# Optimization experiments

Measured on AMD Instinct MI355X. Metric: run time of the kernel, lower is better.

## Reference

```python
import jax, jax.numpy as jnp
import numpy as np
import math

B, T, C, H = 4, 4096, 1024, 16
D = C // H

def setup_inputs() -> dict:
    key = jax.random.key(0)
    k1, k2, k3, k4, k5 = jax.random.split(key, 5)
    s = 1.0 / math.sqrt(C)
    return {
        "x": jax.random.normal(k1, (B, T, C), dtype=jnp.float32),
        "W_qkv": jax.random.normal(k2, (C, 3 * C), dtype=jnp.float32) * s,
        "b_qkv": jax.random.normal(k3, (3 * C,), dtype=jnp.float32) * 0.01,
        "W_out": jax.random.normal(k4, (C, C), dtype=jnp.float32) * s,
        "b_out": jax.random.normal(k5, (C,), dtype=jnp.float32) * 0.01,
    }

def reference(x, W_qkv, b_qkv, W_out, b_out):
    qkv = x @ W_qkv + b_qkv                      # (B,T,3C)
    q, k, v = jnp.split(qkv, 3, axis=2)
    q = q.reshape(B, T, H, D)
    k = k.reshape(B, T, H, D)
    v = v.reshape(B, T, H, D)
    # attention over the HEAD axis per (B,T): scores (B,T,H,H)
    att = jnp.einsum('bthd,btgd->bthg', q, k) / math.sqrt(D)
    att = jax.nn.softmax(att, axis=-1)
    out = jnp.einsum('bthg,btgd->bthd', att, v)  # (B,T,H,D)
    out = out.reshape(B, T, C)
    return out @ W_out + b_out
```

## Files before the change

### kernel.cpp

```cpp
#include <hip/hip_runtime.h>
#include <cstdint>
#include <cstddef>

constexpr int Bc = 4;
constexpr int Tc = 4096;
constexpr int Cc = 1024;
constexpr int Hc = 16;
constexpr int Dc = 64;
constexpr int Mc = Bc * Tc;
constexpr int N1c = 3 * Cc;
constexpr int Kc = Cc;
constexpr int KBc = Kc / 32;

typedef __bf16 bf16x8 __attribute__((ext_vector_type(8)));
typedef float  f32x4  __attribute__((ext_vector_type(4)));
typedef __attribute__((address_space(1))) uint32_t gu32;
typedef __attribute__((address_space(3))) uint32_t lu32;

__device__ __forceinline__ float bf2f(unsigned short u) {
    return __uint_as_float(((unsigned)u) << 16);
}
__device__ __forceinline__ unsigned short f2bf(float f) {
    unsigned u = __float_as_uint(f);
    u += 0x7FFF + ((u >> 16) & 1);
    return (unsigned short)(u >> 16);
}

__device__ __forceinline__ void load_lds16(const void* g, void* l) {
    __builtin_amdgcn_global_load_lds((gu32*)(uintptr_t)g, (lu32*)(uintptr_t)l, 16, 0, 0);
}


__global__ __launch_bounds__(256) void prep_kernel(
    const float* __restrict__ x,    unsigned short* __restrict__ Ap,
    const float* __restrict__ Wqkv, unsigned short* __restrict__ Wqkp,
    const float* __restrict__ Wout, unsigned short* __restrict__ Wop) {
    __shared__ float tile[32][33];
    const int bid = blockIdx.x;
    const int tid = threadIdx.x;

    if (bid < 8192) {
        const int w = tid >> 6, lane = tid & 63;
        const int t = bid * 4 + w;
        const int mb = t >> 5, kb = t & 31;
        const int r = lane >> 2, c = lane & 3;
        const float* src = x + (size_t)(mb * 16 + r) * Kc + kb * 32 + c * 8;
        float4 f0 = *(const float4*)src;
        float4 f1 = *(const float4*)(src + 4);
        unsigned short u[8];
        u[0] = f2bf(f0.x); u[1] = f2bf(f0.y); u[2] = f2bf(f0.z); u[3] = f2bf(f0.w);
        u[4] = f2bf(f1.x); u[5] = f2bf(f1.y); u[6] = f2bf(f1.z); u[7] = f2bf(f1.w);
        *(uint4*)(Ap + (size_t)t * 512 + (c * 16 + r) * 8) = *(uint4*)u;
        return;
    }

    const float* W; unsigned short* Bp; int N; int b2;
    if (bid < 8192 + 3072) { W = Wqkv; Bp = Wqkp; N = 3072; b2 = bid - 8192; }
    else                   { W = Wout; Bp = Wop;  N = 1024; b2 = bid - 11264; }
    const int NT = N >> 5;
    const int n0 = (b2 % NT) * 32, k0 = (b2 / NT) * 32;
    const int tx = tid & 31, ty = tid >> 5;
    for (int i = ty; i < 32; i += 8)
        tile[i][tx] = W[(size_t)(k0 + i) * N + n0 + tx];
    __syncthreads();
    const int t = tid;
    const int h = t >> 7, rr = t & 127, lane = rr >> 1, half = rr & 1;
    const int fq = lane >> 4, fn = lane & 15;
    unsigned short u[4];
    #pragma unroll
    for (int j = 0; j < 4; ++j)
        u[j] = f2bf(tile[fq * 8 + half * 4 + j][h * 16 + fn]);
    size_t tileIdx = (size_t)((n0 >> 4) + h) * (Kc >> 5) + (k0 >> 5);
    *(uint2*)(Bp + tileIdx * 512 + lane * 8 + half * 4) = *(uint2*)u;
}

template <bool OUT_BF16>
__global__ __launch_bounds__(256, 4) void lds_gemm_kernel(
    const unsigned short* __restrict__ Ap,
    const unsigned short* __restrict__ Bp,
    const float* __restrict__ bias,
    void* __restrict__ Cout,
    int M, int N, int K, int NB) {
    __shared__ unsigned short sA[16 * 512];
    __shared__ unsigned short sB[16 * 512];
    const int KB = K >> 5;
    const int MB = M >> 7;
    const int id   = blockIdx.x;
    const int xcd  = id & 7;
    const int per  = id >> 3;
    const int MSTR = MB >> 3;
    const int byl  = per & 7;
    const int bx   = (per >> 3) % NB;
    const int pass = per / (8 * NB);
    const int by   = xcd * MSTR + pass * 8 + byl;

    const int w    = threadIdx.x >> 6;
    const int lane = threadIdx.x & 63;
    const int m0 = by * 128;
    const int n0 = bx * 128;
    const int wm = (w >> 1) * 64;
    const int wn = (w & 1) * 64;

    const unsigned short* gA[4];
    const unsigned short* gB[4];
    unsigned short* lA[4];
    unsigned short* lB[4];
    #pragma unroll
    for (int i = 0; i < 4; ++i) {
        const int t  = w * 4 + i;
        const int mt = t >> 1, s = t & 1;
        gA[i] = Ap + ((size_t)(by * 8 + mt) * KB + s) * 512 + lane * 8;
        gB[i] = Bp + ((size_t)(bx * 8 + mt) * KB + s) * 512 + lane * 8;
        lA[i] = sA + t * 512;
        lB[i] = sB + t * 512;
    }

    const unsigned short* aP = sA + (wm >> 4) * 2 * 512 + lane * 8;
    const unsigned short* bP = sB + (wn >> 4) * 2 * 512 + lane * 8;

    const f32x4 zero4 = {0.f, 0.f, 0.f, 0.f};
    f32x4 acc[4][4];
    #pragma unroll
    for (int i = 0; i < 4; ++i)
        #pragma unroll
        for (int j = 0; j < 4; ++j) acc[i][j] = zero4;

    const int NIT = K >> 6;
    #pragma unroll 1
    for (int jt = 0; jt < NIT; ++jt) {
        #pragma unroll
        for (int i = 0; i < 4; ++i) {
            load_lds16(gA[i], lA[i]);
            load_lds16(gB[i], lB[i]);
        }
        #pragma unroll
        for (int i = 0; i < 4; ++i) { gA[i] += 1024; gB[i] += 1024; }
        __syncthreads();

        #pragma unroll
        for (int kk = 0; kk < 2; ++kk) {
            bf16x8 af[4], bfr[4];
            #pragma unroll
            for (int mi = 0; mi < 4; ++mi)
                af[mi]  = *(const bf16x8*)(aP + (mi * 2 + kk) * 512);
            #pragma unroll
            for (int ni = 0; ni < 4; ++ni)
                bfr[ni] = *(const bf16x8*)(bP + (ni * 2 + kk) * 512);
            #pragma unroll
            for (int mi = 0; mi < 4; ++mi)
                #pragma unroll
                for (int ni = 0; ni < 4; ++ni)
                    acc[mi][ni] = __builtin_amdgcn_mfma_f32_16x16x32_bf16(
                        af[mi], bfr[ni], acc[mi][ni], 0, 0, 0);
        }
        __syncthreads();
    }

    const int fr = lane & 15;
    const int fq = lane >> 4;
    #pragma unroll
    for (int mi = 0; mi < 4; ++mi) {
        #pragma unroll
        for (int ni = 0; ni < 4; ++ni) {
            int row = m0 + wm + mi * 16 + fq * 4;
            int col = n0 + wn + ni * 16 + fr;
            float bb = bias[col];
            #pragma unroll
            for (int r = 0; r < 4; ++r) {
                float v = acc[mi][ni][r] + bb;
                if (OUT_BF16)
                    ((unsigned short*)Cout)[(size_t)(row + r) * N + col] = f2bf(v);
                else
                    ((float*)Cout)[(size_t)(row + r) * N + col] = v;
            }
        }
    }
}

__global__ __launch_bounds__(256) void attn_mfma_kernel(
    const unsigned short* __restrict__ qkv,
    unsigned short* __restrict__ attP) {
    __shared__ char smem[4 * 3584];
    const int w    = threadIdx.x >> 6;
    const int lane = threadIdx.x & 63;
    const int m    = lane & 15;
    const int q    = lane >> 4;
    const int row  = blockIdx.x * 4 + w;
    unsigned short* sV = (unsigned short*)(smem + w * 3584);
    float*          sP = (float*)(smem + w * 3584 + 2304);

    const unsigned short* src = qkv + (size_t)row * 3072;

    bf16x8 aq0 = *(const bf16x8*)(src + m * 64 + q * 8);
    bf16x8 aq1 = *(const bf16x8*)(src + m * 64 + 32 + q * 8);
    bf16x8 bk0 = *(const bf16x8*)(src + 1024 + m * 64 + q * 8);
    bf16x8 bk1 = *(const bf16x8*)(src + 1024 + m * 64 + 32 + q * 8);

    #pragma unroll
    for (int t = 0; t < 2; ++t) {
        int G = t * 64 + lane;
        int r = G >> 3, p = G & 7;
        *(uint4*)(sV + r * 72 + p * 8) = *(const uint4*)(src + 2048 + G * 8);
    }

    f32x4 s = {0.f, 0.f, 0.f, 0.f};
    s = __builtin_amdgcn_mfma_f32_16x16x32_bf16(aq0, bk0, s, 0, 0, 0);
    s = __builtin_amdgcn_mfma_f32_16x16x32_bf16(aq1, bk1, s, 0, 0, 0);

    #pragma unroll
    for (int r = 0; r < 4; ++r) {
        float t0 = s[r] * 0.125f;
        float mx = t0;
        mx = fmaxf(mx, __shfl_xor(mx, 1));
        mx = fmaxf(mx, __shfl_xor(mx, 2));
        mx = fmaxf(mx, __shfl_xor(mx, 4));
        mx = fmaxf(mx, __shfl_xor(mx, 8));
        float e = __expf(t0 - mx);
        float su = e;
        su += __shfl_xor(su, 1);
        su += __shfl_xor(su, 2);
        su += __shfl_xor(su, 4);
        su += __shfl_xor(su, 8);
        sP[(q * 4 + r) * 20 + m] = e / su;
    }
    __syncthreads();

    const float* pr = sP + m * 20 + (q & 1) * 8;
    float4 pf0 = *(const float4*)(pr);
    float4 pf1 = *(const float4*)(pr + 4);
    const bool act = (q < 2);
    union { unsigned short u[8]; bf16x8 b; } pa;
    pa.u[0] = act ? f2bf(pf0.x) : 0;
    pa.u[1] = act ? f2bf(pf0.y) : 0;
    pa.u[2] = act ? f2bf(pf0.z) : 0;
    pa.u[3] = act ? f2bf(pf0.w) : 0;
    pa.u[4] = act ? f2bf(pf1.x) : 0;
    pa.u[5] = act ? f2bf(pf1.y) : 0;
    pa.u[6] = act ? f2bf(pf1.z) : 0;
    pa.u[7] = act ? f2bf(pf1.w) : 0;

    const unsigned short* vb = sV + (q & 1) * 8 * 72;
    const size_t tileBase = (size_t)(row >> 4) * 32 * 512;
    const int fr_tok = row & 15;
    #pragma unroll
    for (int c4 = 0; c4 < 4; ++c4) {
        union { unsigned short u[8]; bf16x8 b; } vf;
        #pragma unroll
        for (int j = 0; j < 8; ++j) vf.u[j] = vb[j * 72 + c4 * 16 + m];
        f32x4 o = {0.f, 0.f, 0.f, 0.f};
        o = __builtin_amdgcn_mfma_f32_16x16x32_bf16(pa.b, vf.b, o, 0, 0, 0);
        #pragma unroll
        for (int r = 0; r < 4; ++r) {
            int col = (q * 4 + r) * 64 + c4 * 16 + m;
            size_t off = tileBase + (size_t)(col >> 5) * 512
                       + (((col >> 3) & 3) * 16 + fr_tok) * 8 + (col & 7);
            attP[off] = f2bf(o[r]);
        }
    }
}

extern "C" void kernel_launch(void* const* d_in, const int* in_sizes, int n_in,
                              void* d_out, int out_size, void* d_ws, size_t ws_size,
                              hipStream_t stream) {
    const float* x    = (const float*)d_in[0];
    const float* Wqkv = (const float*)d_in[1];
    const float* bqkv = (const float*)d_in[2];
    const float* Wout = (const float*)d_in[3];
    const float* bout = (const float*)d_in[4];
    float* out = (float*)d_out;

    char* ws = (char*)d_ws;
    unsigned short* xp   = (unsigned short*)ws;                 ws += (size_t)Mc * Kc * 2;
    unsigned short* Wqkp = (unsigned short*)ws;                 ws += (size_t)N1c * Kc * 2;
    unsigned short* Wop  = (unsigned short*)ws;                 ws += (size_t)Cc * Kc * 2;
    unsigned short* qkv  = (unsigned short*)ws;
    unsigned short* attP = xp;

    prep_kernel<<<8192 + 3072 + 1024, 256, 0, stream>>>(x, xp, Wqkv, Wqkp, Wout, Wop);

    constexpr int Mh = Mc / 2;
    const size_t Ahalf = (size_t)Mh * Kc;
    lds_gemm_kernel<true><<<(N1c / 128) * (Mh / 128), 256, 0, stream>>>(
        xp, Wqkp, bqkv, qkv, Mh, N1c, Kc, N1c / 128);
    lds_gemm_kernel<true><<<(N1c / 128) * (Mh / 128), 256, 0, stream>>>(
        xp + Ahalf, Wqkp, bqkv, qkv + (size_t)Mh * N1c, Mh, N1c, Kc, N1c / 128);

    attn_mfma_kernel<<<Mc / 4, 256, 0, stream>>>(qkv, attP);

    lds_gemm_kernel<false><<<(Cc / 128) * (Mc / 128), 256, 0, stream>>>(
        attP, Wop, bout, out, Mc, Cc, Kc, Cc / 128);
}
```

Baseline: 303.3 us.

## Transpose V in LDS, stage attention output for vector stores, split QKV GEMM by column

The attention kernel now stores V transposed in padded LDS, so each lane reads its MFMA B-fragment with one 16-byte load instead of eight scalar reads. The output tile is staged through LDS and written to the packed attP layout with coalesced 16-byte stores instead of scattered 2-byte stores. The QKV projection is now split into three launches over column thirds (Q, K, V) covering all rows, rather than two launches over row halves. This adds LDS bank-conflict risk on the transposed scatter writes, an extra barrier, and assumes the packed weight layout can be sliced per 1024 columns.

```diff
diff --git a/kernel.cpp b/kernel.cpp
--- a/kernel.cpp
+++ b/kernel.cpp
@@ -180,14 +180,14 @@
 __global__ __launch_bounds__(256) void attn_mfma_kernel(
     const unsigned short* __restrict__ qkv,
     unsigned short* __restrict__ attP) {
-    __shared__ char smem[4 * 3584];
+    __shared__ char smem[4 * 4480];
     const int w    = threadIdx.x >> 6;
     const int lane = threadIdx.x & 63;
     const int m    = lane & 15;
     const int q    = lane >> 4;
     const int row  = blockIdx.x * 4 + w;
-    unsigned short* sV = (unsigned short*)(smem + w * 3584);
-    float*          sP = (float*)(smem + w * 3584 + 2304);
+    unsigned short* sVt = (unsigned short*)(smem + w * 4480);
+    float*          sP  = (float*)(smem + w * 4480 + 3200);
 
     const unsigned short* src = qkv + (size_t)row * 3072;
 
@@ -199,8 +199,12 @@
     #pragma unroll
     for (int t = 0; t < 2; ++t) {
         int G = t * 64 + lane;
-        int r = G >> 3, p = G & 7;
-        *(uint4*)(sV + r * 72 + p * 8) = *(const uint4*)(src + 2048 + G * 8);
+        int g = G >> 3, p = G & 7;
+        uint4 vv = *(const uint4*)(src + 2048 + G * 8);
+        const unsigned short* vs = (const unsigned short*)&vv;
+        #pragma unroll
+        for (int i = 0; i < 8; ++i)
+            sVt[200 * p + 24 * i + g] = vs[i];
     }
 
     f32x4 s = {0.f, 0.f, 0.f, 0.f};
@@ -239,23 +243,37 @@
     pa.u[6] = act ? f2bf(pf1.z) : 0;
     pa.u[7] = act ? f2bf(pf1.w) : 0;
 
-    const unsigned short* vb = sV + (q & 1) * 8 * 72;
+    float o4[4][4];
+    #pragma unroll
+    for (int c4 = 0; c4 < 4; ++c4) {
+        const int d = c4 * 16 + m;
+        bf16x8 vf = *(const bf16x8*)(sVt + d * 24 + (d >> 3) * 8 + (q & 1) * 8);
+        f32x4 o = {0.f, 0.f, 0.f, 0.f};
+        o = __builtin_amdgcn_mfma_f32_16x16x32_bf16(pa.b, vf, o, 0, 0, 0);
+        #pragma unroll
+        for (int r = 0; r < 4; ++r) o4[c4][r] = o[r];
+    }
+    __syncthreads();
+
+    unsigned short* sO = sVt;
+    #pragma unroll
+    for (int c4 = 0; c4 < 4; ++c4) {
+        #pragma unroll
+        for (int r = 0; r < 4; ++r) {
+            int col = (q * 4 + r) * 64 + c4 * 16 + m;
+            sO[col + ((col >> 6) << 3)] = f2bf(o4[c4][r]);
+        }
+    }
+    __syncthreads();
+
     const size_t tileBase = (size_t)(row >> 4) * 32 * 512;
     const int fr_tok = row & 15;
     #pragma unroll
-    for (int c4 = 0; c4 < 4; ++c4) {
-        union { unsigned short u[8]; bf16x8 b; } vf;
-        #pragma unroll
-        for (int j = 0; j < 8; ++j) vf.u[j] = vb[j * 72 + c4 * 16 + m];
-        f32x4 o = {0.f, 0.f, 0.f, 0.f};
-        o = __builtin_amdgcn_mfma_f32_16x16x32_bf16(pa.b, vf.b, o, 0, 0, 0);
-        #pragma unroll
-        for (int r = 0; r < 4; ++r) {
-            int col = (q * 4 + r) * 64 + c4 * 16 + m;
-            size_t off = tileBase + (size_t)(col >> 5) * 512
-                       + (((col >> 3) & 3) * 16 + fr_tok) * 8 + (col & 7);
-            attP[off] = f2bf(o[r]);
-        }
+    for (int t = 0; t < 2; ++t) {
+        int j = t * 64 + lane;
+        uint4 val = *(const uint4*)(sO + j * 8 + ((j >> 3) << 3));
+        *(uint4*)(attP + tileBase + (size_t)(j >> 2) * 512
+                  + ((j & 3) * 16 + fr_tok) * 8) = val;
     }
 }
 
@@ -278,12 +296,11 @@
 
     prep_kernel<<<8192 + 3072 + 1024, 256, 0, stream>>>(x, xp, Wqkv, Wqkp, Wout, Wop);
 
-    constexpr int Mh = Mc / 2;
-    const size_t Ahalf = (size_t)Mh * Kc;
-    lds_gemm_kernel<true><<<(N1c / 128) * (Mh / 128), 256, 0, stream>>>(
-        xp, Wqkp, bqkv, qkv, Mh, N1c, Kc, N1c / 128);
-    lds_gemm_kernel<true><<<(N1c / 128) * (Mh / 128), 256, 0, stream>>>(
-        xp + Ahalf, Wqkp, bqkv, qkv + (size_t)Mh * N1c, Mh, N1c, Kc, N1c / 128);
+    for (int p = 0; p < 3; ++p) {
+        const unsigned short* Bp_p = Wqkp + (size_t)p * 64 * KBc * 512;
+        lds_gemm_kernel<true><<<8 * (Mc / 128), 256, 0, stream>>>(
+            xp, Bp_p, bqkv + p * 1024, qkv + p * 1024, Mc, N1c, Kc, 8);
+    }
 
     attn_mfma_kernel<<<Mc / 4, 256, 0, stream>>>(qkv, attP);
 
```

Measured after the change: 309.0 us. About the same (+1.9%).
